# Optimization experiments

Hardware: AMD Instinct MI355X
Metric: run time of the kernel (lower is better)

## Reference

```python
import jax, jax.numpy as jnp
import numpy as np

N = 65536   # batch_size * timeseries
D = 512     # feature dim of h_real
K = 64      # n_clusters


def setup_inputs() -> dict:
    key = jax.random.key(0)
    k1, k2 = jax.random.split(key)
    h_real = jax.random.normal(k1, (N, D), dtype=jnp.float32)
    # F is an (approximately) orthogonal projection parameter [N, K].
    F = jax.random.normal(k2, (N, K), dtype=jnp.float32)
    return {"h_real": h_real, "F": F}


def reference(h_real, F):
    # Original: WTW = h h^T (N x N); loss = trace(WTW) - trace(F^T WTW F).
    # Algebraically identical reduced form, never materializing the N x N Gram:
    #   trace(h h^T) = sum(h * h)
    #   trace(F^T h h^T F) = ||F^T h||_F^2
    tr_wtw = jnp.sum(h_real * h_real)
    G = F.T @ h_real                      # [K, D] skinny GEMM
    tr_proj = jnp.sum(G * G)
    return tr_wtw - tr_proj
```

## Files before the change

### kernel.cpp

```cpp
#include <hip/hip_runtime.h>
#include <hip/hip_fp16.h>

#define N_TOT 65536
#define D_DIM 512
#define K_DIM 64
#define NC    32
#define HT_S  40
#define GSZ   (K_DIM * D_DIM)

typedef __bf16   bf16x8 __attribute__((ext_vector_type(8)));
typedef float    f32x4  __attribute__((ext_vector_type(4)));
typedef _Float16 half8  __attribute__((ext_vector_type(8)));

__device__ __forceinline__ unsigned int pack_bf16(float a, float b) {
    union { float f; unsigned int u; } x, y;
    x.f = a; y.f = b;
    unsigned int lo = (x.u + 0x7fffu + ((x.u >> 16) & 1u)) >> 16;
    unsigned int hi = (y.u + 0x7fffu + ((y.u >> 16) & 1u)) >> 16;
    return lo | (hi << 16);
}

extern "C" __global__ void __launch_bounds__(1024, 4)
k1_partial(const float* __restrict__ h, const float* __restrict__ F,
           float* __restrict__ trw_out, unsigned short* __restrict__ gpart,
           float* __restrict__ out, int rowsPerBlock) {
    __shared__ unsigned short ht[2][D_DIM * HT_S];
    __shared__ unsigned short Ft[2][K_DIM * HT_S];
    __shared__ float red[16];

    const int tid = threadIdx.x;
    const int b   = blockIdx.x;
    if (b == 0 && tid == 0) out[0] = 0.0f;

    const int row0    = b * rowsPerBlock;
    const int nChunks = rowsPerBlock / NC;

    const int sd = tid & 127;
    const int sg = tid >> 7;
    const int fk = (tid & 15) * 4;
    const int fg = (tid >> 4) & 15;
    const int wave = tid >> 6;
    const int lane = tid & 63;
    const int m    = lane & 15;
    const int q    = lane >> 4;

    f32x4 acc[4][2];
    #pragma unroll
    for (int kt = 0; kt < 4; ++kt)
        #pragma unroll
        for (int dt = 0; dt < 2; ++dt)
            acc[kt][dt] = (f32x4){0.f, 0.f, 0.f, 0.f};

    float trw = 0.f;
    f32x4 v[4];
    f32x4 w0, w1;

    auto issue = [&](int c) {
        const int r0 = row0 + c * NC;
        const float* hb = h + (size_t)(r0 + sg * 4) * D_DIM + sd * 4;
        #pragma unroll
        for (int j = 0; j < 4; ++j)
            v[j] = *(const f32x4*)(hb + (size_t)j * D_DIM);
        if (tid < 256) {
            const float* fb = F + (size_t)(r0 + fg * 2) * K_DIM + fk;
            w0 = *(const f32x4*)fb;
            w1 = *(const f32x4*)(fb + K_DIM);
        }
    };
    auto pack = [&](int p) {
        #pragma unroll
        for (int j = 0; j < 4; ++j)
            #pragma unroll
            for (int e = 0; e < 4; ++e)
                trw += v[j][e] * v[j][e];
        #pragma unroll
        for (int e = 0; e < 4; ++e) {
            uint2 pk;
            pk.x = pack_bf16(v[0][e], v[1][e]);
            pk.y = pack_bf16(v[2][e], v[3][e]);
            *(uint2*)&ht[p][(sd * 4 + e) * HT_S + sg * 4] = pk;
        }
        if (tid < 256) {
            #pragma unroll
            for (int e = 0; e < 4; ++e) {
                unsigned int pk = pack_bf16(w0[e], w1[e]);
                *(unsigned int*)&Ft[p][(fk + e) * HT_S + fg * 2] = pk;
            }
        }
    };

    issue(0); pack(0);

    for (int c = 0; c < nChunks; ++c) {
        __syncthreads();
        const int p = c & 1;

        bf16x8 bfrag[2], afrag[4];
        #pragma unroll
        for (int dt = 0; dt < 2; ++dt)
            bfrag[dt] = *(const bf16x8*)&ht[p][(wave * 32 + dt * 16 + m) * HT_S + q * 8];
        #pragma unroll
        for (int kt = 0; kt < 4; ++kt)
            afrag[kt] = *(const bf16x8*)&Ft[p][(kt * 16 + m) * HT_S + q * 8];

        if (c + 1 < nChunks) issue(c + 1);

        #pragma unroll
        for (int kt = 0; kt < 4; ++kt)
            #pragma unroll
            for (int dt = 0; dt < 2; ++dt)
                acc[kt][dt] = __builtin_amdgcn_mfma_f32_16x16x32_bf16(
                    afrag[kt], bfrag[dt], acc[kt][dt], 0, 0, 0);

        if (c + 1 < nChunks) pack((c + 1) & 1);
    }

    __syncthreads();
    unsigned short* gt = &ht[0][0];
    #pragma unroll
    for (int kt = 0; kt < 4; ++kt)
        #pragma unroll
        for (int dt = 0; dt < 2; ++dt)
            #pragma unroll
            for (int r = 0; r < 4; ++r) {
                const int k = kt * 16 + q * 4 + r;
                const int d = wave * 32 + dt * 16 + m;
                __half hv = __float2half(acc[kt][dt][r]);
                gt[k * D_DIM + d] = *(unsigned short*)&hv;
            }

    #pragma unroll
    for (int off = 32; off > 0; off >>= 1) trw += __shfl_down(trw, off, 64);
    if (lane == 0) red[wave] = trw;
    __syncthreads();

    unsigned short* gp = gpart + (size_t)b * GSZ;
    #pragma unroll
    for (int it = 0; it < 4; ++it)
        *(uint4*)(gp + it * 8192 + tid * 8) = *(const uint4*)(gt + it * 8192 + tid * 8);

    if (tid == 0) {
        float s = 0.f;
        #pragma unroll
        for (int w = 0; w < 16; ++w) s += red[w];
        trw_out[b] = s;
    }
}

extern "C" __global__ void __launch_bounds__(512)
k2_reduce(const float* __restrict__ trw, const unsigned short* __restrict__ gpart,
          float* __restrict__ out, int P) {
    __shared__ float sh[32 * 16 * 8];
    __shared__ float red2[8];

    const int tid = threadIdx.x;
    const int sub = tid >> 4;
    const int oct = tid & 15;
    const int tt  = blockIdx.x * 16 + oct;

    float g[8];
    #pragma unroll
    for (int j = 0; j < 8; ++j) g[j] = 0.f;

    const unsigned short* base = gpart + (size_t)tt * 8;
    for (int b = sub; b < P; b += 32) {
        half8 v = *(const half8*)(base + (size_t)b * GSZ);
        #pragma unroll
        for (int j = 0; j < 8; ++j) g[j] += (float)v[j];
    }
    #pragma unroll
    for (int j = 0; j < 8; ++j) sh[(sub * 16 + oct) * 8 + j] = g[j];
    __syncthreads();

    float val = 0.f;
    if (tid < 128) {
        const int o2 = tid >> 3, j = tid & 7;
        float s = 0.f;
        #pragma unroll
        for (int sb = 0; sb < 32; ++sb) s += sh[(sb * 16 + o2) * 8 + j];
        val = -s * s;
    } else if (blockIdx.x == 0 && tid - 128 < P) {
        val = trw[tid - 128];
    }

    #pragma unroll
    for (int off = 32; off > 0; off >>= 1) val += __shfl_down(val, off, 64);
    if ((tid & 63) == 0) red2[tid >> 6] = val;
    __syncthreads();
    if (tid == 0) {
        float s = 0.f;
        #pragma unroll
        for (int w = 0; w < 8; ++w) s += red2[w];
        atomicAdd(out, s);
    }
}

extern "C" void kernel_launch(void* const* d_in, const int* in_sizes, int n_in,
                              void* d_out, int out_size, void* d_ws, size_t ws_size,
                              hipStream_t stream) {
    const float* h = (const float*)d_in[0];
    const float* F = (const float*)d_in[1];
    float* out = (float*)d_out;

    int P = 256;
    while (P > 1 && (size_t)4096 + (size_t)P * (GSZ * 2) > ws_size) P >>= 1;
    const int rowsPerBlock = N_TOT / P;

    float* trw = (float*)d_ws;
    unsigned short* gpart = (unsigned short*)((char*)d_ws + 4096);

    hipLaunchKernelGGL(k1_partial, dim3(P), dim3(1024), 0, stream,
                       h, F, trw, gpart, out, rowsPerBlock);
    hipLaunchKernelGGL(k2_reduce, dim3(256), dim3(512), 0, stream,
                       trw, gpart, out, P);
}
```

Measured before the change: 212.0 us.

## Load h directly into MFMA B fragments, stage only F in LDS

Removes the LDS transpose staging of h: each lane now reads its B-fragment elements straight from global memory as strided scalar loads and packs them to bf16 in registers. F is staged for 256 rows at a time into a single LDS buffer, so barriers drop to two per 256 rows instead of one per 32 rows. The intent is to cut LDS traffic and synchronisation. The cost is scalar, column-strided global loads of h (16 lanes read consecutive floats, each lane walking rows), which are less coalesced than the previous float4 loads and no longer prefetched one chunk ahead.

```diff
diff --git a/kernel.cpp b/kernel.cpp
--- a/kernel.cpp
+++ b/kernel.cpp
@@ -4,8 +4,7 @@
 #define N_TOT 65536
 #define D_DIM 512
 #define K_DIM 64
-#define NC    32
-#define HT_S  40
+#define FT_S  264
 #define GSZ   (K_DIM * D_DIM)
 
 typedef __bf16   bf16x8 __attribute__((ext_vector_type(8)));
@@ -24,25 +23,19 @@
 k1_partial(const float* __restrict__ h, const float* __restrict__ F,
            float* __restrict__ trw_out, unsigned short* __restrict__ gpart,
            float* __restrict__ out, int rowsPerBlock) {
-    __shared__ unsigned short ht[2][D_DIM * HT_S];
-    __shared__ unsigned short Ft[2][K_DIM * HT_S];
+    __shared__ unsigned short Ft[K_DIM * FT_S];
+    __shared__ unsigned short gt[GSZ];
     __shared__ float red[16];
 
     const int tid = threadIdx.x;
     const int b   = blockIdx.x;
     if (b == 0 && tid == 0) out[0] = 0.0f;
 
-    const int row0    = b * rowsPerBlock;
-    const int nChunks = rowsPerBlock / NC;
-
-    const int sd = tid & 127;
-    const int sg = tid >> 7;
-    const int fk = (tid & 15) * 4;
-    const int fg = (tid >> 4) & 15;
     const int wave = tid >> 6;
     const int lane = tid & 63;
     const int m    = lane & 15;
     const int q    = lane >> 4;
+    const int d0   = wave * 32 + m;
 
     f32x4 acc[4][2];
     #pragma unroll
@@ -52,71 +45,65 @@
             acc[kt][dt] = (f32x4){0.f, 0.f, 0.f, 0.f};
 
     float trw = 0.f;
-    f32x4 v[4];
-    f32x4 w0, w1;
-
-    auto issue = [&](int c) {
-        const int r0 = row0 + c * NC;
-        const float* hb = h + (size_t)(r0 + sg * 4) * D_DIM + sd * 4;
-        #pragma unroll
-        for (int j = 0; j < 4; ++j)
-            v[j] = *(const f32x4*)(hb + (size_t)j * D_DIM);
-        if (tid < 256) {
-            const float* fb = F + (size_t)(r0 + fg * 2) * K_DIM + fk;
-            w0 = *(const f32x4*)fb;
-            w1 = *(const f32x4*)(fb + K_DIM);
+
+    const int nSuper = rowsPerBlock >> 8;
+    for (int sc = 0; sc < nSuper; ++sc) {
+        const int n0 = b * rowsPerBlock + sc * 256;
+
+        if (sc) __syncthreads();
+        {
+            const int fk = (tid & 15) * 4;
+            const int fr = (tid >> 4) & 15;
+            const int sl = tid >> 8;
+            #pragma unroll
+            for (int ss = 0; ss < 2; ++ss) {
+                const int n = (sl + ss * 4) * 32 + fr * 2;
+                const float* fb = F + (size_t)(n0 + n) * K_DIM + fk;
+                f32x4 w0 = *(const f32x4*)fb;
+                f32x4 w1 = *(const f32x4*)(fb + K_DIM);
+                #pragma unroll
+                for (int e = 0; e < 4; ++e)
+                    *(unsigned int*)&Ft[(fk + e) * FT_S + n] = pack_bf16(w0[e], w1[e]);
+            }
         }
-    };
-    auto pack = [&](int p) {
-        #pragma unroll
-        for (int j = 0; j < 4; ++j)
-            #pragma unroll
-            for (int e = 0; e < 4; ++e)
-                trw += v[j][e] * v[j][e];
-        #pragma unroll
-        for (int e = 0; e < 4; ++e) {
-            uint2 pk;
-            pk.x = pack_bf16(v[0][e], v[1][e]);
-            pk.y = pack_bf16(v[2][e], v[3][e]);
-            *(uint2*)&ht[p][(sd * 4 + e) * HT_S + sg * 4] = pk;
+        __syncthreads();
+
+        for (int c = 0; c < 8; ++c) {
+            const int nb = n0 + c * 32 + q * 8;
+            float v[2][8];
+            #pragma unroll
+            for (int dt = 0; dt < 2; ++dt) {
+                const float* hb = h + (size_t)nb * D_DIM + d0 + dt * 16;
+                #pragma unroll
+                for (int j = 0; j < 8; ++j)
+                    v[dt][j] = hb[(size_t)j * D_DIM];
+            }
+            bf16x8 afrag[4];
+            #pragma unroll
+            for (int kt = 0; kt < 4; ++kt)
+                afrag[kt] = *(const bf16x8*)&Ft[(kt * 16 + m) * FT_S + c * 32 + q * 8];
+            bf16x8 bfrag[2];
+            #pragma unroll
+            for (int dt = 0; dt < 2; ++dt) {
+                uint4 pk;
+                pk.x = pack_bf16(v[dt][0], v[dt][1]);
+                pk.y = pack_bf16(v[dt][2], v[dt][3]);
+                pk.z = pack_bf16(v[dt][4], v[dt][5]);
+                pk.w = pack_bf16(v[dt][6], v[dt][7]);
+                bfrag[dt] = *(bf16x8*)&pk;
+                #pragma unroll
+                for (int j = 0; j < 8; ++j)
+                    trw += v[dt][j] * v[dt][j];
+            }
+            #pragma unroll
+            for (int kt = 0; kt < 4; ++kt)
+                #pragma unroll
+                for (int dt = 0; dt < 2; ++dt)
+                    acc[kt][dt] = __builtin_amdgcn_mfma_f32_16x16x32_bf16(
+                        afrag[kt], bfrag[dt], acc[kt][dt], 0, 0, 0);
         }
-        if (tid < 256) {
-            #pragma unroll
-            for (int e = 0; e < 4; ++e) {
-                unsigned int pk = pack_bf16(w0[e], w1[e]);
-                *(unsigned int*)&Ft[p][(fk + e) * HT_S + fg * 2] = pk;
-            }
-        }
-    };
-
-    issue(0); pack(0);
-
-    for (int c = 0; c < nChunks; ++c) {
-        __syncthreads();
-        const int p = c & 1;
-
-        bf16x8 bfrag[2], afrag[4];
-        #pragma unroll
-        for (int dt = 0; dt < 2; ++dt)
-            bfrag[dt] = *(const bf16x8*)&ht[p][(wave * 32 + dt * 16 + m) * HT_S + q * 8];
-        #pragma unroll
-        for (int kt = 0; kt < 4; ++kt)
-            afrag[kt] = *(const bf16x8*)&Ft[p][(kt * 16 + m) * HT_S + q * 8];
-
-        if (c + 1 < nChunks) issue(c + 1);
-
-        #pragma unroll
-        for (int kt = 0; kt < 4; ++kt)
-            #pragma unroll
-            for (int dt = 0; dt < 2; ++dt)
-                acc[kt][dt] = __builtin_amdgcn_mfma_f32_16x16x32_bf16(
-                    afrag[kt], bfrag[dt], acc[kt][dt], 0, 0, 0);
-
-        if (c + 1 < nChunks) pack((c + 1) & 1);
-    }
-
-    __syncthreads();
-    unsigned short* gt = &ht[0][0];
+    }
+
     #pragma unroll
     for (int kt = 0; kt < 4; ++kt)
         #pragma unroll
```

After: 211.1 us. Within noise of the previous version (-0.4%).
